# Kernel optimization log

Measured on AMD Instinct MI355X. Metric: run time of the kernel, lower is better.

## Reference

```python
import jax, jax.numpy as jnp
import numpy as np

CONV1_T = 15.0  # firing threshold of layer 1
CONV2_T = 10.0  # firing threshold of layer 2


def _conv(x, w):
    # valid 2D conv, stride 1, no bias (snn.Convolution)
    return jax.lax.conv_general_dilated(
        x, w, window_strides=(1, 1), padding='VALID',
        dimension_numbers=('NCHW', 'OIHW', 'NCHW'))


def _pad(x, p):
    # sf.pad: zero-pad last two (spatial) dims
    return jnp.pad(x, ((0, 0), (0, 0), (p, p), (p, p)))


def _maxpool(x, k, s):
    # sf.pooling: max_pool2d
    return jax.lax.reduce_window(x, -jnp.inf, jax.lax.max,
                                 (1, 1, k, k), (1, 1, s, s), 'VALID')


def _fire(pot, thr):
    # sf.fire with return_thresholded_potentials=True:
    # F.threshold(pot, thr, 0) then spikes = sign(thresholded)
    pot = jnp.where(pot > thr, pot, jnp.zeros((), pot.dtype))
    return jnp.sign(pot), pot


def setup_inputs() -> dict:
    key = jax.random.key(0)
    k1, k2, k3 = jax.random.split(key, 3)
    # temporally encoded spike input: (T=15, C=6, H=224, W=224)
    inp = jax.random.uniform(k1, (15, 6, 224, 224), dtype=jnp.float32)
    # snn.Convolution weights: normal(mean=0.8, std=0.05)
    w1 = 0.8 + 0.05 * jax.random.normal(k2, (30, 6, 5, 5), dtype=jnp.float32)
    w2 = 0.8 + 0.05 * jax.random.normal(k3, (240, 30, 3, 3), dtype=jnp.float32)
    return {"input": inp, "w1": w1, "w2": w2, "max_layer": 2}


def reference(input, w1, w2, max_layer):
    # eval-mode forward (self.training == False), max_layer == 2
    x = _pad(input, 2)                    # (15,6,228,228)
    pot = _conv(x, w1)                    # (15,30,224,224)
    spk, pot = _fire(pot, CONV1_T)
    if max_layer == 1:
        return spk, pot
    spk_in = _pad(_maxpool(spk, 2, 2), 1)  # (15,30,114,114)
    pot = _conv(spk_in, w2)                # (15,240,112,112)
    spk, pot = _fire(pot, CONV2_T)
    return spk, pot
```

## Files before the change

kernel.cpp:

```cpp
#include <hip/hip_runtime.h>
#include <stdint.h>


typedef _Float16 half8  __attribute__((ext_vector_type(8)));
typedef _Float16 half8u __attribute__((ext_vector_type(8), aligned(4)));
typedef float f32x4  __attribute__((ext_vector_type(4)));
typedef float f32x2  __attribute__((ext_vector_type(2)));

#define POT1_T 15.0f
#define POT2_T 10.0f

#define SPK_ELEMS  (15*114*114*32)
#define SPK_BYTES  (SPK_ELEMS*2)
#define BP2_OFF    SPK_BYTES
#define BP2_BYTES  (9*15*64*8*2)
#define BP1_OFF    (BP2_OFF + BP2_BYTES)
#define BP1_BYTES  (8*2*64*8*2)
#define IN16_OFF   (BP1_OFF + BP1_BYTES)
#define IN16_ELEMS (90*228*228)

#define PAD_BLOCKS ((IN16_ELEMS + 255) / 256)
#define RING_ELEMS (15*452*32)
#define RING_BLOCKS ((RING_ELEMS + 255) / 256)

__device__ __forceinline__ unsigned short f2h(float v) {
  union { _Float16 h; unsigned short u; } c;
  c.h = (_Float16)v;
  return c.u;
}

__global__ __launch_bounds__(256) void prep(
    const float* __restrict__ in, const float* __restrict__ w1,
    const float* __restrict__ w2, unsigned short* __restrict__ ina,
    unsigned short* __restrict__ bp2, unsigned short* __restrict__ bp1,
    unsigned short* __restrict__ spk16)
{
  const int blk = blockIdx.x;
  if (blk < PAD_BLOCKS) {
    const int i = blk * 256 + threadIdx.x;
    if (i >= IN16_ELEMS) return;
    const int xx = i % 228, t = i / 228;
    const int yy = t % 228, c = t / 228;
    const int xi = xx - 2, yi = yy - 2;
    float v = 0.0f;
    if ((unsigned)xi < 224u && (unsigned)yi < 224u)
      v = in[(c * 224 + yi) * 224 + xi];
    const unsigned short h = f2h(v);
    unsigned short* inb = ina + IN16_ELEMS;
    ina[i] = h;
    if (i > 0) inb[i - 1] = h;
    if (i == IN16_ELEMS - 1) inb[i] = 0;
    return;
  }
  if (blk < PAD_BLOCKS + RING_BLOCKS) {
    const int i = (blk - PAD_BLOCKS) * 256 + threadIdx.x;
    if (i >= RING_ELEMS) return;
    const int ch = i & 31, t = i >> 5;
    const int p = t % 452, n = t / 452;
    int y, x;
    if (p < 114)      { y = 0;       x = p; }
    else if (p < 228) { y = 113;     x = p - 114; }
    else if (p < 340) { y = p - 227; x = 0; }
    else              { y = p - 339; x = 113; }
    spk16[((size_t)(n * 114 + y) * 114 + x) * 32 + ch] = 0;
    return;
  }
  if (threadIdx.x >= 64) return;
  const int b = blk - PAD_BLOCKS - RING_BLOCKS;
  const int lane = threadIdx.x;
  const int quad = lane >> 4, nl = lane & 15;
  if (b < 135) {
    const int s = b / 15, nsub = b - s * 15;
    const int ch = nsub * 16 + nl;
    unsigned short* dst = bp2 + (((s * 15 + nsub) * 64 + lane) << 3);
    #pragma unroll
    for (int j = 0; j < 8; ++j) {
      const int ci = quad * 8 + j;
      dst[j] = f2h((ci < 30) ? w2[ch * 270 + ci * 9 + s] : 0.0f);
    }
  } else {
    const int bb = b - 135;
    const int s = bb >> 1, nsub = bb & 1;
    const int ch = nsub * 16 + nl;
    unsigned short* dst = bp1 + (((s * 2 + nsub) * 64 + lane) << 3);
    #pragma unroll
    for (int j = 0; j < 8; ++j) {
      int ci, ky;
      bool ok = (ch < 30) && (j < 5);
      if (s < 6)       { ci = s;        ky = quad; }
      else if (s == 6) { ci = quad;     ky = 4;    }
      else             { ci = 4 + quad; ky = 4; ok = ok && (quad < 2); }
      float v = 0.0f;
      if (ok) v = w1[ch * 150 + ci * 25 + ky * 5 + j];
      dst[j] = f2h(v);
    }
  }
}

__global__ __launch_bounds__(256) void conv1_mfma(
    const unsigned short* __restrict__ in16,
    const unsigned short* __restrict__ bp1,
    unsigned short* __restrict__ spk16)
{
  const int tid = threadIdx.x;
  const int wave = tid >> 6, lane = tid & 63;
  const int quad = lane >> 4, nl = lane & 15;
  const int m0 = blockIdx.x * 256 + wave * 64;

  const unsigned short* base = in16 + ((nl & 1) ? (IN16_ELEMS - 1) : 0);

  unsigned o_q[4], o_a[4], o_b[4];
  #pragma unroll
  for (int c = 0; c < 4; ++c) {
    const int m = m0 + c * 16 + nl;
    const int sub = m & 3, g = m >> 2;
    const int gx = g % 112, t = g / 112;
    const int gy = t % 112, n = t / 112;
    const int y0 = gy * 2 + (sub >> 1);
    const int x0 = gx * 2 + (sub & 1);
    const unsigned nb = (unsigned)n * 311904u;
    o_q[c] = nb + (unsigned)((y0 + quad) * 228 + x0);
    o_a[c] = nb + (unsigned)quad * 51984u + (unsigned)((y0 + 4) * 228 + x0);
    o_b[c] = nb + (unsigned)(4 + (quad & 1)) * 51984u + (unsigned)((y0 + 4) * 228 + x0);
  }

  f32x4 acc[4][2];
  #pragma unroll
  for (int c = 0; c < 4; ++c) {
    acc[c][0] = (f32x4){0.f, 0.f, 0.f, 0.f};
    acc[c][1] = (f32x4){0.f, 0.f, 0.f, 0.f};
  }

  const half8* bptr = (const half8*)bp1;
  #pragma unroll
  for (int s = 0; s < 8; ++s) {
    const half8 b0 = bptr[(s * 2 + 0) * 64 + lane];
    const half8 b1 = bptr[(s * 2 + 1) * 64 + lane];
    #pragma unroll
    for (int c = 0; c < 4; ++c) {
      const unsigned off = (s < 6) ? (o_q[c] + (unsigned)s * 51984u)
                                   : (s == 6 ? o_a[c] : o_b[c]);
      const half8 A = *(const half8u*)(base + off);
      acc[c][0] = __builtin_amdgcn_mfma_f32_16x16x32_f16(A, b0, acc[c][0], 0, 0, 0);
      acc[c][1] = __builtin_amdgcn_mfma_f32_16x16x32_f16(A, b1, acc[c][1], 0, 0, 0);
    }
  }

  #pragma unroll
  for (int c = 0; c < 4; ++c) {
    const int gq = ((m0 + c * 16) >> 2) + quad;
    const int pgx = gq % 112, tq = gq / 112;
    const int pgy = tq % 112, nq = tq / 112;
    const bool f0 = (acc[c][0][0] > POT1_T) | (acc[c][0][1] > POT1_T) |
                    (acc[c][0][2] > POT1_T) | (acc[c][0][3] > POT1_T);
    const bool f1 = (acc[c][1][0] > POT1_T) | (acc[c][1][1] > POT1_T) |
                    (acc[c][1][2] > POT1_T) | (acc[c][1][3] > POT1_T);
    const size_t o = ((size_t)(nq * 114 + pgy + 1) * 114 + (pgx + 1)) * 32 + nl;
    spk16[o] = f0 ? (unsigned short)0x3C00 : (unsigned short)0;
    spk16[o + 16] = (nl < 14 && f1) ? (unsigned short)0x3C00 : (unsigned short)0;
  }
}

#define C2_NSUB 5
#define TPAD 258
__global__ __launch_bounds__(256, 3) void conv2_mfma(
    const unsigned short* __restrict__ spk16,
    const unsigned short* __restrict__ bp2,
    float* __restrict__ out_spk, float* __restrict__ out_pot)
{
  __shared__ __attribute__((aligned(16))) unsigned short Blds[C2_NSUB * 9 * 64 * 8];

  const int tid = threadIdx.x;
  const int ntile = blockIdx.y;
  for (int i = tid; i < 2880; i += 256) {
    const int su = i / 576, rem = i - su * 576;
    ((uint4*)Blds)[su * 576 + rem] =
        ((const uint4*)bp2)[((rem >> 6) * 15 + ntile * C2_NSUB + su) * 64 + (rem & 63)];
  }
  __syncthreads();

  const int wave = tid >> 6, lane = tid & 63;
  const int quad = lane >> 4, nl = lane & 15;
  const int bx = blockIdx.x;
  const int m0 = bx * 256 + wave * 64;

  const unsigned short* abase[4];
  #pragma unroll
  for (int c = 0; c < 4; ++c) {
    const int m = m0 + c * 16 + nl;
    const int x = m % 112, t = m / 112;
    const int y = t % 112, n = t / 112;
    abase[c] = spk16 + ((size_t)(n * 114 + y) * 114 + x) * 32 + quad * 8;
  }

  f32x4 acc[4][C2_NSUB];
  #pragma unroll
  for (int c = 0; c < 4; ++c)
    #pragma unroll
    for (int u = 0; u < C2_NSUB; ++u) acc[c][u] = (f32x4){0.f, 0.f, 0.f, 0.f};

  const half8* blds = (const half8*)Blds;
  #pragma unroll
  for (int s = 0; s < 9; ++s) {
    const int ky = s / 3, kx = s - ky * 3;
    half8 a[4];
    #pragma unroll
    for (int c = 0; c < 4; ++c)
      a[c] = *(const half8*)(abase[c] + (ky * 114 + kx) * 32);
    #pragma unroll
    for (int u = 0; u < C2_NSUB; ++u) {
      const half8 b = blds[(u * 9 + s) * 64 + lane];
      #pragma unroll
      for (int c = 0; c < 4; ++c)
        acc[c][u] = __builtin_amdgcn_mfma_f32_16x16x32_f16(a[c], b, acc[c][u], 0, 0, 0);
    }
  }

  float* T = (float*)Blds;
  const int n   = (bx * 256) / 12544;
  const int ip0 = (bx * 256) % 12544;
  const size_t obase = (size_t)n * 240 * 12544 + ip0 + 4 * lane;

  #pragma unroll
  for (int u = 0; u < C2_NSUB; ++u) {
    __syncthreads();
    #pragma unroll
    for (int c = 0; c < 4; ++c) {
      const int mb = wave * 64 + c * 16 + quad * 4;
      #pragma unroll
      for (int rr = 0; rr < 4; ++rr)
        T[nl * TPAD + mb + rr] = acc[c][u][rr];
    }
    __syncthreads();
    #pragma unroll
    for (int j = 0; j < 4; ++j) {
      const int chl = wave * 4 + j;
      const int ch  = (ntile * C2_NSUB + u) * 16 + chl;
      const f32x2 lo = *(const f32x2*)&T[chl * TPAD + 4 * lane];
      const f32x2 hi = *(const f32x2*)&T[chl * TPAD + 4 * lane + 2];
      f32x4 pt, sp;
      pt[0] = lo[0]; pt[1] = lo[1]; pt[2] = hi[0]; pt[3] = hi[1];
      #pragma unroll
      for (int rr = 0; rr < 4; ++rr) {
        const bool f = pt[rr] > POT2_T;
        sp[rr] = f ? 1.0f : 0.0f;
        pt[rr] = f ? pt[rr] : 0.0f;
      }
      const size_t o = obase + (size_t)ch * 12544;
      *(f32x4*)(out_spk + o) = sp;
      *(f32x4*)(out_pot + o) = pt;
    }
  }
}

extern "C" void kernel_launch(void* const* d_in, const int* in_sizes, int n_in,
                              void* d_out, int out_size, void* d_ws, size_t ws_size,
                              hipStream_t stream)
{
  const float* in = (const float*)d_in[0];
  const float* w1 = (const float*)d_in[1];
  const float* w2 = (const float*)d_in[2];
  float* out = (float*)d_out;

  unsigned short* spk16 = (unsigned short*)d_ws;
  unsigned short* bp2   = (unsigned short*)((char*)d_ws + BP2_OFF);
  unsigned short* bp1   = (unsigned short*)((char*)d_ws + BP1_OFF);
  unsigned short* ina   = (unsigned short*)((char*)d_ws + IN16_OFF);

  prep<<<PAD_BLOCKS + RING_BLOCKS + 151, 256, 0, stream>>>(
      in, w1, w2, ina, bp2, bp1, spk16);
  conv1_mfma<<<2940, 256, 0, stream>>>(ina, bp1, spk16);
  conv2_mfma<<<dim3(735, 3), 256, 0, stream>>>(
      spk16, bp2, out, out + (size_t)15 * 240 * 112 * 112);
}
```

Baseline: 132.6 us.

## Stage conv2 input spike rows in LDS with swizzle, read weights from global

The conv2 kernel now copies the block's spike-input rows (up to six padded rows) into shared memory, using an XOR swizzle to avoid bank conflicts. The 3x3 taps are then read from LDS rather than straight from global memory. Weights, which used to be staged in LDS, are now loaded directly from global memory on every MFMA step. The aim is to cut redundant global reads of overlapping input windows, in exchange for more global weight traffic and an LDS sized for six rows. Note that 256 pixels can span four image rows, which need six rows once the kernel halo is included.

```diff
diff --git a/kernel.cpp b/kernel.cpp
--- a/kernel.cpp
+++ b/kernel.cpp
@@ -162,35 +162,48 @@
 }
 
 #define C2_NSUB 5
+#define NROWS 6
 #define TPAD 258
 __global__ __launch_bounds__(256, 3) void conv2_mfma(
     const unsigned short* __restrict__ spk16,
     const unsigned short* __restrict__ bp2,
     float* __restrict__ out_spk, float* __restrict__ out_pot)
 {
-  __shared__ __attribute__((aligned(16))) unsigned short Blds[C2_NSUB * 9 * 64 * 8];
+  __shared__ __attribute__((aligned(16))) unsigned short As[NROWS * 114 * 32];
 
   const int tid = threadIdx.x;
   const int ntile = blockIdx.y;
-  for (int i = tid; i < 2880; i += 256) {
-    const int su = i / 576, rem = i - su * 576;
-    ((uint4*)Blds)[su * 576 + rem] =
-        ((const uint4*)bp2)[((rem >> 6) * 15 + ntile * C2_NSUB + su) * 64 + (rem & 63)];
+  const int bx = blockIdx.x;
+  const int mimg = bx * 256;
+  const int n   = mimg / 12544;
+  const int ip0 = mimg % 12544;
+  const int y0  = ip0 / 112;
+
+  {
+    const int nrows = (114 - y0 < NROWS) ? (114 - y0) : NROWS;
+    const uint4* src = (const uint4*)(spk16 + ((size_t)(n * 114 + y0) * 114) * 32);
+    uint4* dst = (uint4*)As;
+    for (int i = tid; i < nrows * 456; i += 256) {
+      const int g = i % 456, r = i / 456;
+      const int d = (g & ~3) | ((g & 3) ^ ((g >> 2) & 3));
+      dst[r * 456 + d] = src[i];
+    }
   }
   __syncthreads();
 
   const int wave = tid >> 6, lane = tid & 63;
   const int quad = lane >> 4, nl = lane & 15;
-  const int bx = blockIdx.x;
-  const int m0 = bx * 256 + wave * 64;
-
-  const unsigned short* abase[4];
-  #pragma unroll
-  for (int c = 0; c < 4; ++c) {
-    const int m = m0 + c * 16 + nl;
-    const int x = m % 112, t = m / 112;
-    const int y = t % 112, n = t / 112;
-    abase[c] = spk16 + ((size_t)(n * 114 + y) * 114 + x) * 32 + quad * 8;
+
+  int bo[4], swz[4][3];
+  #pragma unroll
+  for (int c = 0; c < 4; ++c) {
+    const int widx = wave * 64 + c * 16 + nl;
+    const int x  = (ip0 + widx) % 112;
+    const int yl = (ip0 + widx) / 112 - y0;
+    bo[c] = (yl * 114 + x) * 64;
+    #pragma unroll
+    for (int k = 0; k < 3; ++k)
+      swz[c][k] = (quad ^ ((x + k) & 3)) << 4;
   }
 
   f32x4 acc[4][C2_NSUB];
@@ -199,26 +212,25 @@
     #pragma unroll
     for (int u = 0; u < C2_NSUB; ++u) acc[c][u] = (f32x4){0.f, 0.f, 0.f, 0.f};
 
-  const half8* blds = (const half8*)Blds;
+  const char* asb = (const char*)As;
+  const half8* bgl = (const half8*)bp2;
   #pragma unroll
   for (int s = 0; s < 9; ++s) {
     const int ky = s / 3, kx = s - ky * 3;
     half8 a[4];
     #pragma unroll
     for (int c = 0; c < 4; ++c)
-      a[c] = *(const half8*)(abase[c] + (ky * 114 + kx) * 32);
+      a[c] = *(const half8*)(asb + (bo[c] + (ky * 114 + kx) * 64 + swz[c][kx]));
     #pragma unroll
     for (int u = 0; u < C2_NSUB; ++u) {
-      const half8 b = blds[(u * 9 + s) * 64 + lane];
+      const half8 b = bgl[(s * 15 + ntile * C2_NSUB + u) * 64 + lane];
       #pragma unroll
       for (int c = 0; c < 4; ++c)
         acc[c][u] = __builtin_amdgcn_mfma_f32_16x16x32_f16(a[c], b, acc[c][u], 0, 0, 0);
     }
   }
 
-  float* T = (float*)Blds;
-  const int n   = (bx * 256) / 12544;
-  const int ip0 = (bx * 256) % 12544;
+  float* T = (float*)As;
   const size_t obase = (size_t)n * 240 * 12544 + ip0 + 4 * lane;
 
   #pragma unroll
```

Measured after the change: 150.1 us. +13.2%, slower.
